# Optimization experiments

Hardware: AMD Instinct MI355X
Metric: run time of the kernel (lower is better)

Reference implementation:

```python
import jax, jax.numpy as jnp
import numpy as np

EPS = 1e-12  # torch F.normalize clamp_min eps
NUM_HEADS = 4


def setup_inputs() -> dict:
    key = jax.random.key(0)
    ks = jax.random.split(key, 6)
    B, N, C = 8, 8192, 256
    x1 = jax.random.normal(ks[0], (B, N, C), dtype=jnp.float32)
    x2 = jax.random.normal(ks[1], (B, N, C), dtype=jnp.float32)
    s = 1.0 / np.sqrt(C)
    Wq = jax.random.normal(ks[2], (C, C), dtype=jnp.float32) * s
    Wk = jax.random.normal(ks[3], (C, C), dtype=jnp.float32) * s
    Wv = jax.random.normal(ks[4], (C, C), dtype=jnp.float32) * s
    Wo = jax.random.normal(ks[5], (C, C), dtype=jnp.float32) * s
    bo = jnp.zeros((C,), dtype=jnp.float32)
    temperature = jnp.ones((NUM_HEADS, 1, 1), dtype=jnp.float32)
    return {"x1": x1, "x2": x2, "Wq": Wq, "Wk": Wk, "Wv": Wv,
            "Wo": Wo, "bo": bo, "temperature": temperature}


def reference(x1, x2, Wq, Wk, Wv, Wo, bo, temperature):
    B, N, C = x1.shape
    H = NUM_HEADS
    d = C // H
    # Linear projections (torch Linear: y = x W^T), then [B,H,d,N] layout
    q = (x1 @ Wq.T).reshape(B, N, H, d).transpose(0, 2, 3, 1)  # [B,H,d,N]
    k = (x2 @ Wk.T).reshape(B, N, H, d).transpose(0, 2, 3, 1)  # [B,H,d,N]
    v = (x2 @ Wv.T).reshape(B, N, H, d).transpose(0, 2, 3, 1)  # [B,H,d,N]
    # L2-normalize along the token axis (dim=-1)
    qn = q / jnp.maximum(jnp.linalg.norm(q, axis=-1, keepdims=True), EPS)
    kn = k / jnp.maximum(jnp.linalg.norm(k, axis=-1, keepdims=True), EPS)
    # Channel-wise cross-covariance attention: [B,H,d,d]
    attn = jnp.einsum('bhdn,bhen->bhde', qn, kn) * temperature
    attn = jax.nn.softmax(attn, axis=-1)
    # (dropout is identity in eval mode)
    x_cross = jnp.einsum('bhde,bhen->bhdn', attn, v)  # [B,H,d,N]
    x_cross = x_cross.transpose(0, 3, 1, 2).reshape(B, N, C)  # [B,N,C]
    return x_cross @ Wo.T + bo
```

## Files before the change

kernel.cpp:

```cpp
#include <hip/hip_runtime.h>
#include <hip/hip_bf16.h>

#define BDIM 8
#define NTOK 8192
#define CDIM 256
#define HEADS 4
#define DHEAD 64
#define MROWS (BDIM * NTOK)

typedef unsigned short ushort_t;
typedef short bf16x8 __attribute__((ext_vector_type(8)));
typedef float f32x4 __attribute__((ext_vector_type(4)));
typedef unsigned short u16x8 __attribute__((ext_vector_type(8)));
typedef unsigned short u16x4 __attribute__((ext_vector_type(4)));

__device__ inline ushort_t f2bf(float f) {
    __hip_bfloat16 h = __float2bfloat16(f);
    return *reinterpret_cast<ushort_t*>(&h);
}

__device__ inline u16x8 pack8(float4 a, float4 b) {
    u16x8 o;
    o[0] = f2bf(a.x); o[1] = f2bf(a.y); o[2] = f2bf(a.z); o[3] = f2bf(a.w);
    o[4] = f2bf(b.x); o[5] = f2bf(b.y); o[6] = f2bf(b.z); o[7] = f2bf(b.w);
    return o;
}

__global__ __launch_bounds__(256) void zero_kernel(float* __restrict__ p, int n) {
    int i = blockIdx.x * 256 + threadIdx.x;
    if (i < n) p[i] = 0.0f;
}

__global__ __launch_bounds__(256) void proj_mfma(
    const float* __restrict__ x1, const float* __restrict__ x2,
    const float* __restrict__ Wq, const float* __restrict__ Wk,
    const float* __restrict__ Wv,
    ushort_t* __restrict__ qp, ushort_t* __restrict__ kp, ushort_t* __restrict__ vp,
    float* __restrict__ ssq, float* __restrict__ ssk)
{
    const float* A; const float* W; ushort_t* outp; float* ss;
    if (blockIdx.z == 0)      { A = x1; W = Wq; outp = qp; ss = ssq; }
    else if (blockIdx.z == 1) { A = x2; W = Wk; outp = kp; ss = ssk; }
    else                      { A = x2; W = Wv; outp = vp; ss = nullptr; }

    __shared__ ushort_t Asl[2][4096];
    __shared__ ushort_t Bsl[2][4096];
    __shared__ float colss[128];

    const int t = threadIdx.x;
    const int lane = t & 63, w = t >> 6;
    const int l16 = lane & 15, quad = lane >> 4;
    const int m0 = blockIdx.x * 128, c0 = blockIdx.y * 128;
    const int wm = (w >> 1) * 64, wn = (w & 1) * 64;

    const int srow = t >> 1;
    const int skh  = t & 1;

    const float* Ap = A + (size_t)(m0 + srow) * CDIM + skh * 16;
    const float* Wp = W + (size_t)(c0 + srow) * CDIM + skh * 16;

    float4 ga[4], gb[4];
#pragma unroll
    for (int i = 0; i < 4; ++i) {
        ga[i] = *(const float4*)(Ap + i * 4);
        gb[i] = *(const float4*)(Wp + i * 4);
    }

    f32x4 acc[4][4] = {};

#pragma unroll 2
    for (int it = 0; it < 8; ++it) {
        ushort_t* As = Asl[it & 1];
        ushort_t* Bs = Bsl[it & 1];
        *(u16x8*)&As[(skh * 2 + 0) * 1024 + srow * 8] = pack8(ga[0], ga[1]);
        *(u16x8*)&As[(skh * 2 + 1) * 1024 + srow * 8] = pack8(ga[2], ga[3]);
        *(u16x8*)&Bs[(skh * 2 + 0) * 1024 + srow * 8] = pack8(gb[0], gb[1]);
        *(u16x8*)&Bs[(skh * 2 + 1) * 1024 + srow * 8] = pack8(gb[2], gb[3]);
        if (it < 7) {
            int ko = (it + 1) * 32;
#pragma unroll
            for (int i = 0; i < 4; ++i) {
                ga[i] = *(const float4*)(Ap + ko + i * 4);
                gb[i] = *(const float4*)(Wp + ko + i * 4);
            }
        }
        asm volatile("s_waitcnt lgkmcnt(0)" ::: "memory");
        __builtin_amdgcn_s_barrier();
        bf16x8 aF[4], bF[4];
#pragma unroll
        for (int i = 0; i < 4; ++i)
            aF[i] = *(const bf16x8*)&As[quad * 1024 + (wm + i * 16 + l16) * 8];
#pragma unroll
        for (int j = 0; j < 4; ++j)
            bF[j] = *(const bf16x8*)&Bs[quad * 1024 + (wn + j * 16 + l16) * 8];
#pragma unroll
        for (int i = 0; i < 4; ++i)
#pragma unroll
            for (int j = 0; j < 4; ++j)
                acc[i][j] = __builtin_amdgcn_mfma_f32_16x16x32_bf16(aF[i], bF[j], acc[i][j], 0, 0, 0);
    }

#pragma unroll
    for (int i = 0; i < 4; ++i) {
#pragma unroll
        for (int j = 0; j < 4; ++j) {
            int col = c0 + wn + j * 16 + l16;
#pragma unroll
            for (int reg = 0; reg < 4; ++reg) {
                int row = m0 + wm + i * 16 + quad * 4 + reg;
                outp[(size_t)row * CDIM + col] = f2bf(acc[i][j][reg]);
            }
        }
    }

    if (ss) {
        __syncthreads();
        if (t < 128) colss[t] = 0.0f;
        __syncthreads();
#pragma unroll
        for (int j = 0; j < 4; ++j) {
            float s = 0.0f;
#pragma unroll
            for (int i = 0; i < 4; ++i)
#pragma unroll
                for (int reg = 0; reg < 4; ++reg)
                    s += acc[i][j][reg] * acc[i][j][reg];
            atomicAdd(&colss[wn + j * 16 + l16], s);
        }
        __syncthreads();
        if (t < 128) {
            int b = m0 >> 13;
            atomicAdd(&ss[b * CDIM + c0 + t], colss[t]);
        }
    }
}

__global__ __launch_bounds__(256) void gram_mfma(
    const ushort_t* __restrict__ qp, const ushort_t* __restrict__ kp,
    float* __restrict__ G)
{
    constexpr int NS = 144;
    __shared__ ushort_t qs[64 * NS];
    __shared__ ushort_t ks2[64 * NS];
    __shared__ float gsum[4096];

    const int t = threadIdx.x;
    const int lane = t & 63, w = t >> 6;
    const int l16 = lane & 15, quad = lane >> 4;
    const int slab = blockIdx.x, h = blockIdx.y, b = blockIdx.z;
    const size_t base = (size_t)b * NTOK * CDIM + h * DHEAD;

    const int cg  = t >> 5;
    const int ng4 = t & 31;

    for (int i = t; i < 4096; i += 256) gsum[i] = 0.0f;

    f32x4 acc[4][4] = {};

    for (int n0 = slab * 512; n0 < slab * 512 + 512; n0 += 128) {
        u16x8 qv[4], kv[4];
#pragma unroll
        for (int i = 0; i < 4; ++i) {
            size_t g = base + (size_t)(n0 + ng4 * 4 + i) * CDIM + cg * 8;
            qv[i] = *(const u16x8*)&qp[g];
            kv[i] = *(const u16x8*)&kp[g];
        }
        __syncthreads();
#pragma unroll
        for (int j = 0; j < 8; ++j) {
            u16x4 wq, wk;
            wq[0] = qv[0][j]; wq[1] = qv[1][j]; wq[2] = qv[2][j]; wq[3] = qv[3][j];
            wk[0] = kv[0][j]; wk[1] = kv[1][j]; wk[2] = kv[2][j]; wk[3] = kv[3][j];
            *(u16x4*)&qs[(cg * 8 + j) * NS + ng4 * 4] = wq;
            *(u16x4*)&ks2[(cg * 8 + j) * NS + ng4 * 4] = wk;
        }
        __syncthreads();
        bf16x8 aF[4], bF[4];
#pragma unroll
        for (int i = 0; i < 4; ++i)
            aF[i] = *(const bf16x8*)&qs[(i * 16 + l16) * NS + w * 32 + quad * 8];
#pragma unroll
        for (int j = 0; j < 4; ++j)
            bF[j] = *(const bf16x8*)&ks2[(j * 16 + l16) * NS + w * 32 + quad * 8];
#pragma unroll
        for (int i = 0; i < 4; ++i)
#pragma unroll
            for (int j = 0; j < 4; ++j)
                acc[i][j] = __builtin_amdgcn_mfma_f32_16x16x32_bf16(aF[i], bF[j], acc[i][j], 0, 0, 0);
    }

    __syncthreads();
#pragma unroll
    for (int i = 0; i < 4; ++i)
#pragma unroll
        for (int j = 0; j < 4; ++j)
#pragma unroll
            for (int reg = 0; reg < 4; ++reg)
                atomicAdd(&gsum[(i * 16 + quad * 4 + reg) * 64 + j * 16 + l16], acc[i][j][reg]);
    __syncthreads();

    float* Gp = G + (size_t)(b * HEADS + h) * 4096;
    for (int i = t; i < 4096; i += 256) atomicAdd(&Gp[i], gsum[i]);
}

__global__ __launch_bounds__(64) void attn_softmax(
    float* __restrict__ G, const float* __restrict__ ssq,
    const float* __restrict__ ssk, const float* __restrict__ temp)
{
    const int h = blockIdx.x, b = blockIdx.y;
    const int d = threadIdx.x;
    __shared__ float nk[64];

    float nq = fmaxf(sqrtf(ssq[b * CDIM + h * DHEAD + d]), 1e-12f);
    nk[d]    = fmaxf(sqrtf(ssk[b * CDIM + h * DHEAD + d]), 1e-12f);
    __syncthreads();

    float* row = G + (size_t)(b * HEADS + h) * DHEAD * DHEAD + d * DHEAD;
    const float tmp = temp[h];

    float vals[64];
    float mx = -1e30f;
#pragma unroll
    for (int e = 0; e < 64; ++e) {
        float v = row[e] / (nq * nk[e]) * tmp;
        vals[e] = v;
        mx = fmaxf(mx, v);
    }
    float s = 0.0f;
#pragma unroll
    for (int e = 0; e < 64; ++e) {
        float ev = __expf(vals[e] - mx);
        vals[e] = ev;
        s += ev;
    }
    float inv = 1.0f / s;
#pragma unroll
    for (int e = 0; e < 64; ++e) row[e] = vals[e] * inv;
}

__global__ __launch_bounds__(256) void weff_kernel(
    const float* __restrict__ Wo, const float* __restrict__ attn,
    ushort_t* __restrict__ Weffb)
{
    const int h = blockIdx.x, b = blockIdx.y;
    const int c = threadIdx.x;
    __shared__ float at[64][65];

    const float* Ab = attn + (size_t)(b * HEADS + h) * DHEAD * DHEAD;
    for (int idx = c; idx < DHEAD * DHEAD; idx += 256)
        at[idx >> 6][idx & 63] = Ab[idx];
    __syncthreads();

    float wo[64];
#pragma unroll
    for (int d2 = 0; d2 < 64; ++d2) wo[d2] = Wo[(size_t)c * CDIM + h * DHEAD + d2];

    ushort_t* Wb = Weffb + (size_t)b * CDIM * CDIM + (size_t)c * CDIM + h * DHEAD;
#pragma unroll 4
    for (int e = 0; e < 64; ++e) {
        float s = 0.0f;
#pragma unroll
        for (int d2 = 0; d2 < 64; ++d2) s += wo[d2] * at[d2][e];
        Wb[e] = f2bf(s);
    }
}

__global__ __launch_bounds__(256) void out_mfma(
    const ushort_t* __restrict__ vp, const ushort_t* __restrict__ Weffb,
    const float* __restrict__ bo, float* __restrict__ out)
{
    __shared__ ushort_t Asl[2][4096];
    __shared__ ushort_t Bsl[2][4096];

    const int t = threadIdx.x;
    const int lane = t & 63, w = t >> 6;
    const int l16 = lane & 15, quad = lane >> 4;
    const int m0 = blockIdx.x * 128, c0 = blockIdx.y * 128;
    const int wm = (w >> 1) * 64, wn = (w & 1) * 64;

    const int srow = t >> 1;
    const int skh  = t & 1;

    const ushort_t* Ap = vp + (size_t)(m0 + srow) * CDIM + skh * 16;
    const ushort_t* Bp = Weffb + (size_t)(m0 >> 13) * CDIM * CDIM
                       + (size_t)(c0 + srow) * CDIM + skh * 16;

    u16x8 ga0 = *(const u16x8*)Ap,       ga1 = *(const u16x8*)(Ap + 8);
    u16x8 gb0 = *(const u16x8*)Bp,       gb1 = *(const u16x8*)(Bp + 8);

    f32x4 acc[4][4] = {};

#pragma unroll 2
    for (int it = 0; it < 8; ++it) {
        ushort_t* As = Asl[it & 1];
        ushort_t* Bs = Bsl[it & 1];
        *(u16x8*)&As[(skh * 2 + 0) * 1024 + srow * 8] = ga0;
        *(u16x8*)&As[(skh * 2 + 1) * 1024 + srow * 8] = ga1;
        *(u16x8*)&Bs[(skh * 2 + 0) * 1024 + srow * 8] = gb0;
        *(u16x8*)&Bs[(skh * 2 + 1) * 1024 + srow * 8] = gb1;
        if (it < 7) {
            int ko = (it + 1) * 32;
            ga0 = *(const u16x8*)(Ap + ko);
            ga1 = *(const u16x8*)(Ap + ko + 8);
            gb0 = *(const u16x8*)(Bp + ko);
            gb1 = *(const u16x8*)(Bp + ko + 8);
        }
        asm volatile("s_waitcnt lgkmcnt(0)" ::: "memory");
        __builtin_amdgcn_s_barrier();
        bf16x8 aF[4], bF[4];
#pragma unroll
        for (int i = 0; i < 4; ++i)
            aF[i] = *(const bf16x8*)&As[quad * 1024 + (wm + i * 16 + l16) * 8];
#pragma unroll
        for (int j = 0; j < 4; ++j)
            bF[j] = *(const bf16x8*)&Bs[quad * 1024 + (wn + j * 16 + l16) * 8];
#pragma unroll
        for (int i = 0; i < 4; ++i)
#pragma unroll
            for (int j = 0; j < 4; ++j)
                acc[i][j] = __builtin_amdgcn_mfma_f32_16x16x32_bf16(aF[i], bF[j], acc[i][j], 0, 0, 0);
    }

#pragma unroll
    for (int i = 0; i < 4; ++i) {
#pragma unroll
        for (int j = 0; j < 4; ++j) {
            int col = c0 + wn + j * 16 + l16;
            float bias = bo[col];
#pragma unroll
            for (int reg = 0; reg < 4; ++reg) {
                int row = m0 + wm + i * 16 + quad * 4 + reg;
                out[(size_t)row * CDIM + col] = acc[i][j][reg] + bias;
            }
        }
    }
}

extern "C" void kernel_launch(void* const* d_in, const int* in_sizes, int n_in,
                              void* d_out, int out_size, void* d_ws, size_t ws_size,
                              hipStream_t stream) {
    const float* x1   = (const float*)d_in[0];
    const float* x2   = (const float*)d_in[1];
    const float* Wq   = (const float*)d_in[2];
    const float* Wk   = (const float*)d_in[3];
    const float* Wv   = (const float*)d_in[4];
    const float* Wo   = (const float*)d_in[5];
    const float* bo   = (const float*)d_in[6];
    const float* temp = (const float*)d_in[7];
    float* out = (float*)d_out;

    char* ws = (char*)d_ws;
    const size_t SZP = (size_t)MROWS * CDIM * sizeof(ushort_t);
    ushort_t* qp   = (ushort_t*)(ws);
    ushort_t* kp   = (ushort_t*)(ws + SZP);
    ushort_t* vp   = (ushort_t*)(ws + 2 * SZP);
    float*    ssq  = (float*)(ws + 3 * SZP);
    float*    ssk  = (float*)(ws + 3 * SZP + 8192);
    float*    G    = (float*)(ws + 3 * SZP + 16384);
    ushort_t* Weffb= (ushort_t*)(ws + 3 * SZP + 540672);

    zero_kernel<<<dim3((135168 + 255) / 256), dim3(256), 0, stream>>>(ssq, 135168);

    proj_mfma<<<dim3(MROWS / 128, CDIM / 128, 3), dim3(256), 0, stream>>>(
        x1, x2, Wq, Wk, Wv, qp, kp, vp, ssq, ssk);

    gram_mfma<<<dim3(16, HEADS, BDIM), dim3(256), 0, stream>>>(qp, kp, G);

    attn_softmax<<<dim3(HEADS, BDIM), dim3(64), 0, stream>>>(G, ssq, ssk, temp);

    weff_kernel<<<dim3(HEADS, BDIM), dim3(256), 0, stream>>>(Wo, G, Weffb);

    out_mfma<<<dim3(MROWS / 128, CDIM / 128), dim3(256), 0, stream>>>(vp, Weffb, bo, out);
}
```

Baseline: 350.9 us.

## Pre-convert weights, stage full weight slab in LDS, write transposed Q/K for gram

Adds a kernel that converts Wq/Wk/Wv to bf16 once. The projection and output GEMMs now hold the whole 128x256 weight slab in padded LDS and stream activation fragments straight from global memory into MFMA operands, with no per-k-step A staging. The projection also writes Q and K in a transposed [B,H,d,N] layout through an LDS transpose, so the gram kernel can load MFMA fragments directly from global memory without its LDS transpose. The intent is to remove LDS traffic and barriers from the main loops. The cost is non-coalesced, direct global loads for A fragments, plus extra LDS use that limits occupancy.

```diff
diff --git a/kernel.cpp b/kernel.cpp
--- a/kernel.cpp
+++ b/kernel.cpp
@@ -7,6 +7,8 @@
 #define HEADS 4
 #define DHEAD 64
 #define MROWS (BDIM * NTOK)
+#define WS_STRIDE 264
+#define TS_STRIDE 136
 
 typedef unsigned short ushort_t;
 typedef short bf16x8 __attribute__((ext_vector_type(8)));
@@ -19,10 +21,12 @@
     return *reinterpret_cast<ushort_t*>(&h);
 }
 
-__device__ inline u16x8 pack8(float4 a, float4 b) {
-    u16x8 o;
-    o[0] = f2bf(a.x); o[1] = f2bf(a.y); o[2] = f2bf(a.z); o[3] = f2bf(a.w);
-    o[4] = f2bf(b.x); o[5] = f2bf(b.y); o[6] = f2bf(b.z); o[7] = f2bf(b.w);
+__device__ inline bf16x8 pack8(float4 a, float4 b) {
+    bf16x8 o;
+    o[0] = (short)f2bf(a.x); o[1] = (short)f2bf(a.y);
+    o[2] = (short)f2bf(a.z); o[3] = (short)f2bf(a.w);
+    o[4] = (short)f2bf(b.x); o[5] = (short)f2bf(b.y);
+    o[6] = (short)f2bf(b.z); o[7] = (short)f2bf(b.w);
     return o;
 }
 
@@ -31,157 +35,161 @@
     if (i < n) p[i] = 0.0f;
 }
 
-__global__ __launch_bounds__(256) void proj_mfma(
+__global__ __launch_bounds__(256) void cvt_w(
+    const float* __restrict__ Wq, const float* __restrict__ Wk,
+    const float* __restrict__ Wv, ushort_t* __restrict__ Wb3)
+{
+    int i = (blockIdx.x * 256 + threadIdx.x) * 8;
+    const float* s; int off;
+    if (i < 65536)       { s = Wq; off = i; }
+    else if (i < 131072) { s = Wk; off = i - 65536; }
+    else                 { s = Wv; off = i - 131072; }
+    float4 a = *(const float4*)&s[off];
+    float4 b = *(const float4*)&s[off + 4];
+    *(bf16x8*)&Wb3[i] = pack8(a, b);
+}
+
+__global__ __launch_bounds__(256, 2) void proj_direct(
     const float* __restrict__ x1, const float* __restrict__ x2,
-    const float* __restrict__ Wq, const float* __restrict__ Wk,
-    const float* __restrict__ Wv,
-    ushort_t* __restrict__ qp, ushort_t* __restrict__ kp, ushort_t* __restrict__ vp,
+    const ushort_t* __restrict__ Wb3,
+    ushort_t* __restrict__ qT, ushort_t* __restrict__ kT,
+    ushort_t* __restrict__ vp,
     float* __restrict__ ssq, float* __restrict__ ssk)
 {
-    const float* A; const float* W; ushort_t* outp; float* ss;
-    if (blockIdx.z == 0)      { A = x1; W = Wq; outp = qp; ss = ssq; }
-    else if (blockIdx.z == 1) { A = x2; W = Wk; outp = kp; ss = ssk; }
-    else                      { A = x2; W = Wv; outp = vp; ss = nullptr; }
-
-    __shared__ ushort_t Asl[2][4096];
-    __shared__ ushort_t Bsl[2][4096];
+    __shared__ ushort_t Ws[128 * WS_STRIDE];
     __shared__ float colss[128];
 
     const int t = threadIdx.x;
     const int lane = t & 63, w = t >> 6;
     const int l16 = lane & 15, quad = lane >> 4;
-    const int m0 = blockIdx.x * 128, c0 = blockIdx.y * 128;
-    const int wm = (w >> 1) * 64, wn = (w & 1) * 64;
-
-    const int srow = t >> 1;
-    const int skh  = t & 1;
-
-    const float* Ap = A + (size_t)(m0 + srow) * CDIM + skh * 16;
-    const float* Wp = W + (size_t)(c0 + srow) * CDIM + skh * 16;
-
-    float4 ga[4], gb[4];
-#pragma unroll
-    for (int i = 0; i < 4; ++i) {
-        ga[i] = *(const float4*)(Ap + i * 4);
-        gb[i] = *(const float4*)(Wp + i * 4);
-    }
-
-    f32x4 acc[4][4] = {};
+    const int zc = blockIdx.x;
+    const int z = zc >> 1, c0 = (zc & 1) * 128;
+    const int m0 = blockIdx.y * 128;
+    const int b = m0 >> 13;
+    const int nloc = m0 & (NTOK - 1);
+
+    const float* A = (z == 0) ? x1 : x2;
+    const ushort_t* W = Wb3 + z * 65536;
+
+    {
+        const int c = t >> 1, kh = t & 1;
+        const ushort_t* src = W + (size_t)(c0 + c) * CDIM + kh * 128;
+        ushort_t* dst = &Ws[c * WS_STRIDE + kh * 128];
+#pragma unroll
+        for (int r = 0; r < 16; ++r)
+            *(u16x8*)&dst[r * 8] = *(const u16x8*)&src[r * 8];
+    }
+    __syncthreads();
+
+    const int wm = w * 32;
+    const size_t arow0 = (size_t)(m0 + wm + l16) * CDIM;
+
+    f32x4 acc[2][8] = {};
 
 #pragma unroll 2
     for (int it = 0; it < 8; ++it) {
-        ushort_t* As = Asl[it & 1];
-        ushort_t* Bs = Bsl[it & 1];
-        *(u16x8*)&As[(skh * 2 + 0) * 1024 + srow * 8] = pack8(ga[0], ga[1]);
-        *(u16x8*)&As[(skh * 2 + 1) * 1024 + srow * 8] = pack8(ga[2], ga[3]);
-        *(u16x8*)&Bs[(skh * 2 + 0) * 1024 + srow * 8] = pack8(gb[0], gb[1]);
-        *(u16x8*)&Bs[(skh * 2 + 1) * 1024 + srow * 8] = pack8(gb[2], gb[3]);
-        if (it < 7) {
-            int ko = (it + 1) * 32;
-#pragma unroll
-            for (int i = 0; i < 4; ++i) {
-                ga[i] = *(const float4*)(Ap + ko + i * 4);
-                gb[i] = *(const float4*)(Wp + ko + i * 4);
+        const int kk = it * 32 + quad * 8;
+        bf16x8 aF[2];
+#pragma unroll
+        for (int i = 0; i < 2; ++i) {
+            float4 lo = *(const float4*)&A[arow0 + (size_t)i * 16 * CDIM + kk];
+            float4 hi = *(const float4*)&A[arow0 + (size_t)i * 16 * CDIM + kk + 4];
+            aF[i] = pack8(lo, hi);
+        }
+        bf16x8 bF[8];
+#pragma unroll
+        for (int j = 0; j < 8; ++j)
+            bF[j] = *(const bf16x8*)&Ws[(j * 16 + l16) * WS_STRIDE + kk];
+#pragma unroll
+        for (int i = 0; i < 2; ++i)
+#pragma unroll
+            for (int j = 0; j < 8; ++j)
+                acc[i][j] = __builtin_amdgcn_mfma_f32_16x16x32_bf16(aF[i], bF[j], acc[i][j], 0, 0, 0);
+    }
+
+    if (z == 2) {
+#pragma unroll
+        for (int i = 0; i < 2; ++i)
+#pragma unroll
+            for (int j = 0; j < 8; ++j) {
+                int colg = c0 + j * 16 + l16;
+#pragma unroll
+                for (int reg = 0; reg < 4; ++reg) {
+                    int row = m0 + wm + i * 16 + quad * 4 + reg;
+                    vp[(size_t)row * CDIM + colg] = f2bf(acc[i][j][reg]);
+                }
             }
+        return;
+    }
+
+    float* ss = (z == 0) ? ssq : ssk;
+    ushort_t* T = (z == 0) ? qT : kT;
+
+    __syncthreads();
+    if (t < 128) colss[t] = 0.0f;
+    ushort_t* Ts = Ws;
+#pragma unroll
+    for (int i = 0; i < 2; ++i)
+#pragma unroll
+        for (int j = 0; j < 8; ++j) {
+            u16x4 p;
+            p[0] = f2bf(acc[i][j][0]); p[1] = f2bf(acc[i][j][1]);
+            p[2] = f2bf(acc[i][j][2]); p[3] = f2bf(acc[i][j][3]);
+            *(u16x4*)&Ts[(j * 16 + l16) * TS_STRIDE + wm + i * 16 + quad * 4] = p;
         }
-        asm volatile("s_waitcnt lgkmcnt(0)" ::: "memory");
-        __builtin_amdgcn_s_barrier();
-        bf16x8 aF[4], bF[4];
-#pragma unroll
-        for (int i = 0; i < 4; ++i)
-            aF[i] = *(const bf16x8*)&As[quad * 1024 + (wm + i * 16 + l16) * 8];
-#pragma unroll
-        for (int j = 0; j < 4; ++j)
-            bF[j] = *(const bf16x8*)&Bs[quad * 1024 + (wn + j * 16 + l16) * 8];
-#pragma unroll
-        for (int i = 0; i < 4; ++i)
-#pragma unroll
-            for (int j = 0; j < 4; ++j)
-                acc[i][j] = __builtin_amdgcn_mfma_f32_16x16x32_bf16(aF[i], bF[j], acc[i][j], 0, 0, 0);
-    }
-
-#pragma unroll
-    for (int i = 0; i < 4; ++i) {
-#pragma unroll
-        for (int j = 0; j < 4; ++j) {
-            int col = c0 + wn + j * 16 + l16;
-#pragma unroll
-            for (int reg = 0; reg < 4; ++reg) {
-                int row = m0 + wm + i * 16 + quad * 4 + reg;
-                outp[(size_t)row * CDIM + col] = f2bf(acc[i][j][reg]);
-            }
-        }
-    }
-
-    if (ss) {
-        __syncthreads();
-        if (t < 128) colss[t] = 0.0f;
-        __syncthreads();
-#pragma unroll
-        for (int j = 0; j < 4; ++j) {
-            float s = 0.0f;
-#pragma unroll
-            for (int i = 0; i < 4; ++i)
-#pragma unroll
-                for (int reg = 0; reg < 4; ++reg)
-                    s += acc[i][j][reg] * acc[i][j][reg];
-            atomicAdd(&colss[wn + j * 16 + l16], s);
-        }
-        __syncthreads();
-        if (t < 128) {
-            int b = m0 >> 13;
-            atomicAdd(&ss[b * CDIM + c0 + t], colss[t]);
-        }
-    }
-}
-
-__global__ __launch_bounds__(256) void gram_mfma(
-    const ushort_t* __restrict__ qp, const ushort_t* __restrict__ kp,
+    __syncthreads();
+
+#pragma unroll
+    for (int j = 0; j < 8; ++j) {
+        float s = 0.0f;
+#pragma unroll
+        for (int i = 0; i < 2; ++i)
+#pragma unroll
+            for (int reg = 0; reg < 4; ++reg)
+                s += acc[i][j][reg] * acc[i][j][reg];
+        atomicAdd(&colss[j * 16 + l16], s);
+    }
+
+    {
+        const int r = t >> 1, mh = t & 1;
+        const int cg = c0 + r;
+        const int h = cg >> 6, d = cg & 63;
+        ushort_t* dst = T + ((size_t)(b * HEADS + h) * 64 + d) * NTOK + nloc + mh * 64;
+#pragma unroll
+        for (int u = 0; u < 8; ++u)
+            *(u16x8*)&dst[u * 8] = *(const u16x8*)&Ts[r * TS_STRIDE + mh * 64 + u * 8];
+    }
+    __syncthreads();
+    if (t < 128) atomicAdd(&ss[b * CDIM + c0 + t], colss[t]);
+}
+
+__global__ __launch_bounds__(256) void gram_direct(
+    const ushort_t* __restrict__ qT, const ushort_t* __restrict__ kT,
     float* __restrict__ G)
 {
-    constexpr int NS = 144;
-    __shared__ ushort_t qs[64 * NS];
-    __shared__ ushort_t ks2[64 * NS];
     __shared__ float gsum[4096];
 
     const int t = threadIdx.x;
     const int lane = t & 63, w = t >> 6;
     const int l16 = lane & 15, quad = lane >> 4;
-    const int slab = blockIdx.x, h = blockIdx.y, b = blockIdx.z;
-    const size_t base = (size_t)b * NTOK * CDIM + h * DHEAD;
-
-    const int cg  = t >> 5;
-    const int ng4 = t & 31;
+    const int slab = blockIdx.x, bh = blockIdx.y;
+    const ushort_t* Qb = qT + (size_t)bh * 64 * NTOK;
+    const ushort_t* Kb = kT + (size_t)bh * 64 * NTOK;
 
     for (int i = t; i < 4096; i += 256) gsum[i] = 0.0f;
 
     f32x4 acc[4][4] = {};
 
-    for (int n0 = slab * 512; n0 < slab * 512 + 512; n0 += 128) {
-        u16x8 qv[4], kv[4];
-#pragma unroll
-        for (int i = 0; i < 4; ++i) {
-            size_t g = base + (size_t)(n0 + ng4 * 4 + i) * CDIM + cg * 8;
-            qv[i] = *(const u16x8*)&qp[g];
-            kv[i] = *(const u16x8*)&kp[g];
-        }
-        __syncthreads();
-#pragma unroll
-        for (int j = 0; j < 8; ++j) {
-            u16x4 wq, wk;
-            wq[0] = qv[0][j]; wq[1] = qv[1][j]; wq[2] = qv[2][j]; wq[3] = qv[3][j];
-            wk[0] = kv[0][j]; wk[1] = kv[1][j]; wk[2] = kv[2][j]; wk[3] = kv[3][j];
-            *(u16x4*)&qs[(cg * 8 + j) * NS + ng4 * 4] = wq;
-            *(u16x4*)&ks2[(cg * 8 + j) * NS + ng4 * 4] = wk;
-        }
-        __syncthreads();
+#pragma unroll
+    for (int r = 0; r < 4; ++r) {
+        const int n_off = slab * 512 + r * 128 + w * 32 + quad * 8;
         bf16x8 aF[4], bF[4];
 #pragma unroll
         for (int i = 0; i < 4; ++i)
-            aF[i] = *(const bf16x8*)&qs[(i * 16 + l16) * NS + w * 32 + quad * 8];
+            aF[i] = *(const bf16x8*)&Qb[(size_t)(i * 16 + l16) * NTOK + n_off];
 #pragma unroll
         for (int j = 0; j < 4; ++j)
-            bF[j] = *(const bf16x8*)&ks2[(j * 16 + l16) * NS + w * 32 + quad * 8];
+            bF[j] = *(const bf16x8*)&Kb[(size_t)(j * 16 + l16) * NTOK + n_off];
 #pragma unroll
         for (int i = 0; i < 4; ++i)
 #pragma unroll
@@ -199,7 +207,7 @@
                 atomicAdd(&gsum[(i * 16 + quad * 4 + reg) * 64 + j * 16 + l16], acc[i][j][reg]);
     __syncthreads();
 
-    float* Gp = G + (size_t)(b * HEADS + h) * 4096;
+    float* Gp = G + (size_t)bh * 4096;
     for (int i = t; i < 4096; i += 256) atomicAdd(&Gp[i], gsum[i]);
 }
 
@@ -265,75 +273,65 @@
     }
 }
 
-__global__ __launch_bounds__(256) void out_mfma(
+__global__ __launch_bounds__(256, 2) void out_direct(
     const ushort_t* __restrict__ vp, const ushort_t* __restrict__ Weffb,
     const float* __restrict__ bo, float* __restrict__ out)
 {
-    __shared__ ushort_t Asl[2][4096];
-    __shared__ ushort_t Bsl[2][4096];
+    __shared__ ushort_t Ws[128 * WS_STRIDE];
 
     const int t = threadIdx.x;
     const int lane = t & 63, w = t >> 6;
     const int l16 = lane & 15, quad = lane >> 4;
-    const int m0 = blockIdx.x * 128, c0 = blockIdx.y * 128;
-    const int wm = (w >> 1) * 64, wn = (w & 1) * 64;
-
-    const int srow = t >> 1;
-    const int skh  = t & 1;
-
-    const ushort_t* Ap = vp + (size_t)(m0 + srow) * CDIM + skh * 16;
-    const ushort_t* Bp = Weffb + (size_t)(m0 >> 13) * CDIM * CDIM
-                       + (size_t)(c0 + srow) * CDIM + skh * 16;
-
-    u16x8 ga0 = *(const u16x8*)Ap,       ga1 = *(const u16x8*)(Ap + 8);
-    u16x8 gb0 = *(const u16x8*)Bp,       gb1 = *(const u16x8*)(Bp + 8);
-
-    f32x4 acc[4][4] = {};
+    const int c0 = blockIdx.x * 128;
+    const int m0 = blockIdx.y * 128;
+    const int b = m0 >> 13;
+    const ushort_t* Wb = Weffb + (size_t)b * CDIM * CDIM;
+
+    {
+        const int c = t >> 1, kh = t & 1;
+        const ushort_t* src = Wb + (size_t)(c0 + c) * CDIM + kh * 128;
+        ushort_t* dst = &Ws[c * WS_STRIDE + kh * 128];
+#pragma unroll
+        for (int r = 0; r < 16; ++r)
+            *(u16x8*)&dst[r * 8] = *(const u16x8*)&src[r * 8];
+    }
+    __syncthreads();
+
+    const int wm = w * 32;
+    const size_t arow0 = (size_t)(m0 + wm + l16) * CDIM;
+
+    f32x4 acc[2][8] = {};
 
 #pragma unroll 2
     for (int it = 0; it < 8; ++it) {
-        ushort_t* As = Asl[it & 1];
-        ushort_t* Bs = Bsl[it & 1];
-        *(u16x8*)&As[(skh * 2 + 0) * 1024 + srow * 8] = ga0;
-        *(u16x8*)&As[(skh * 2 + 1) * 1024 + srow * 8] = ga1;
-        *(u16x8*)&Bs[(skh * 2 + 0) * 1024 + srow * 8] = gb0;
-        *(u16x8*)&Bs[(skh * 2 + 1) * 1024 + srow * 8] = gb1;
-        if (it < 7) {
-            int ko = (it + 1) * 32;
-            ga0 = *(const u16x8*)(Ap + ko);
-            ga1 = *(const u16x8*)(Ap + ko + 8);
-            gb0 = *(const u16x8*)(Bp + ko);
-            gb1 = *(const u16x8*)(Bp + ko + 8);
-        }
-        asm volatile("s_waitcnt lgkmcnt(0)" ::: "memory");
-        __builtin_amdgcn_s_barrier();
-        bf16x8 aF[4], bF[4];
-#pragma unroll
-        for (int i = 0; i < 4; ++i)
-            aF[i] = *(const bf16x8*)&As[quad * 1024 + (wm + i * 16 + l16) * 8];
-#pragma unroll
-        for (int j = 0; j < 4; ++j)
-            bF[j] = *(const bf16x8*)&Bs[quad * 1024 + (wn + j * 16 + l16) * 8];
-#pragma unroll
-        for (int i = 0; i < 4; ++i)
-#pragma unroll
-            for (int j = 0; j < 4; ++j)
+        const int kk = it * 32 + quad * 8;
+        bf16x8 aF[2];
+#pragma unroll
+        for (int i = 0; i < 2; ++i)
+            aF[i] = *(const bf16x8*)&vp[arow0 + (size_t)i * 16 * CDIM + kk];
+        bf16x8 bF[8];
+#pragma unroll
+        for (int j = 0; j < 8; ++j)
+            bF[j] = *(const bf16x8*)&Ws[(j * 16 + l16) * WS_STRIDE + kk];
+#pragma unroll
+        for (int i = 0; i < 2; ++i)
+#pragma unroll
+            for (int j = 0; j < 8; ++j)
                 acc[i][j] = __builtin_amdgcn_mfma_f32_16x16x32_bf16(aF[i], bF[j], acc[i][j], 0, 0, 0);
     }
 
 #pragma unroll
-    for (int i = 0; i < 4; ++i) {
-#pragma unroll
-        for (int j = 0; j < 4; ++j) {
-            int col = c0 + wn + j * 16 + l16;
-            float bias = bo[col];
+    for (int i = 0; i < 2; ++i)
+#pragma unroll
+        for (int j = 0; j < 8; ++j) {
+            int colg = c0 + j * 16 + l16;
+            float bias = bo[colg];
 #pragma unroll
             for (int reg = 0; reg < 4; ++reg) {
                 int row = m0 + wm + i * 16 + quad * 4 + reg;
-                out[(size_t)row * CDIM + col] = acc[i][j][reg] + bias;
+                out[(size_t)row * CDIM + colg] = acc[i][j][reg] + bias;
             }
         }
-    }
 }
 
 extern "C" void kernel_launch(void* const* d_in, const int* in_sizes, int n_in,
@@ -351,24 +349,27 @@
 
     char* ws = (char*)d_ws;
     const size_t SZP = (size_t)MROWS * CDIM * sizeof(ushort_t);
-    ushort_t* qp   = (ushort_t*)(ws);
-    ushort_t* kp   = (ushort_t*)(ws + SZP);
+    ushort_t* qT   = (ushort_t*)(ws);
+    ushort_t* kT   = (ushort_t*)(ws + SZP);
     ushort_t* vp   = (ushort_t*)(ws + 2 * SZP);
     float*    ssq  = (float*)(ws + 3 * SZP);
     float*    ssk  = (float*)(ws + 3 * SZP + 8192);
     float*    G    = (float*)(ws + 3 * SZP + 16384);
     ushort_t* Weffb= (ushort_t*)(ws + 3 * SZP + 540672);
+    ushort_t* Wb3  = (ushort_t*)(ws + 3 * SZP + 1589248);
 
     zero_kernel<<<dim3((135168 + 255) / 256), dim3(256), 0, stream>>>(ssq, 135168);
 
-    proj_mfma<<<dim3(MROWS / 128, CDIM / 128, 3), dim3(256), 0, stream>>>(
-        x1, x2, Wq, Wk, Wv, qp, kp, vp, ssq, ssk);
-
-    gram_mfma<<<dim3(16, HEADS, BDIM), dim3(256), 0, stream>>>(qp, kp, G);
+    cvt_w<<<dim3(96), dim3(256), 0, stream>>>(Wq, Wk, Wv, Wb3);
+
+    proj_direct<<<dim3(6, 512), dim3(256), 0, stream>>>(
+        x1, x2, Wb3, qT, kT, vp, ssq, ssk);
+
+    gram_direct<<<dim3(16, 32), dim3(256), 0, stream>>>(qT, kT, G);
 
     attn_softmax<<<dim3(HEADS, BDIM), dim3(64), 0, stream>>>(G, ssq, ssk, temp);
 
     weff_kernel<<<dim3(HEADS, BDIM), dim3(256), 0, stream>>>(Wo, G, Weffb);
 
-    out_mfma<<<dim3(MROWS / 128, CDIM / 128), dim3(256), 0, stream>>>(vp, Weffb, bo, out);
-}
+    out_direct<<<dim3(2, 512), dim3(256), 0, stream>>>(vp, Weffb, bo, out);
+}
```

Result: slower. 385.9 us (+10.0%).
